# Kernel optimization log

Hardware: AMD Instinct MI355X
Metric: run time of the kernel (lower is better)

The kernel has to match this reference:

```python
import jax, jax.numpy as jnp
import numpy as np

VOCAB = 50257
D_EMB = 128
HIDDEN = 256
N_CLS = 2
B, T = 256, 2048


def setup_inputs() -> dict:
    key = jax.random.key(0)
    ks = jax.random.split(key, 8)
    batch = jax.random.randint(ks[0], (B, T), 0, VOCAB, dtype=jnp.int64) if jax.config.jax_enable_x64 else jax.random.randint(ks[0], (B, T), 0, VOCAB, dtype=jnp.int32)
    emb_table = jax.random.normal(ks[1], (VOCAB, D_EMB), dtype=jnp.float32) * 0.02
    emb_table = emb_table.at[0].set(0.0)  # padding_idx=0
    sx = 1.0 / np.sqrt(D_EMB)
    sh = 1.0 / np.sqrt(HIDDEN)
    wx_w = jax.random.uniform(ks[2], (D_EMB, HIDDEN), jnp.float32, -sx, sx)
    wx_b = jax.random.uniform(ks[3], (HIDDEN,), jnp.float32, -sx, sx)
    wh_w = jax.random.uniform(ks[4], (HIDDEN, HIDDEN), jnp.float32, -sh, sh)
    wh_b = jax.random.uniform(ks[5], (HIDDEN,), jnp.float32, -sh, sh)
    clf_w = jax.random.uniform(ks[6], (HIDDEN, N_CLS), jnp.float32, -sh, sh)
    clf_b = jax.random.uniform(ks[7], (N_CLS,), jnp.float32, -sh, sh)
    return {"batch": batch, "emb_table": emb_table, "wx_w": wx_w, "wx_b": wx_b,
            "wh_w": wh_w, "wh_b": wh_b, "clf_w": clf_w, "clf_b": clf_b}


def reference(batch, emb_table, wx_w, wx_b, wh_w, wh_b, clf_w, clf_b):
    # emb: [B, T, D_EMB]
    emb = emb_table[batch]
    b, t, d = emb.shape
    h0 = jnp.zeros((b, wh_w.shape[0]), dtype=emb.dtype)
    # Precompute wx(x) for all timesteps in one big GEMM (same math,
    # hoists the time-invariant contraction out of the sequential loop).
    ax = jnp.einsum('btd,dh->bth', emb, wx_w) + wx_b  # [B, T, H]

    def step(h, a_t):
        h_new = jnp.tanh(a_t + h @ wh_w + wh_b)
        return h_new, None

    h_final, _ = jax.lax.scan(step, h0, jnp.swapaxes(ax, 0, 1))  # scan over T
    return h_final @ clf_w + clf_b  # [B, 2]
```

## Files before the change

kernel.cpp:

```cpp
#include <hip/hip_runtime.h>
#include <hip/hip_bf16.h>

#define VOCAB  50257
#define D_EMB  128
#define HID    256
#define N_CLS  2
#define BSZ    256
#define T_LEN  2048

__global__ __launch_bounds__(256)
void tabax_kernel(const float* __restrict__ emb,
                  const float* __restrict__ wxw,
                  const float* __restrict__ wxb,
                  const float* __restrict__ whb,
                  float* __restrict__ tab)
{
    const int j  = threadIdx.x;
    const int v0 = blockIdx.x * 32;
    const int rows = min(32, VOCAB - v0);

    __shared__ float ebuf[32 * D_EMB];
    for (int i = j; i < rows * D_EMB; i += 256)
        ebuf[i] = emb[(size_t)v0 * D_EMB + i];
    __syncthreads();

    float acc[32];
#pragma unroll
    for (int r = 0; r < 32; ++r) acc[r] = 0.f;

#pragma unroll 8
    for (int d = 0; d < D_EMB; ++d) {
        float wxv = wxw[d * HID + j];
#pragma unroll
        for (int r = 0; r < 32; ++r)
            acc[r] = fmaf(ebuf[r * D_EMB + d], wxv, acc[r]);
    }

    const float bb = wxb[j] + whb[j];
    for (int r = 0; r < rows; ++r)
        tab[(size_t)(v0 + r) * HID + j] = acc[r] + bb;
}

__device__ __forceinline__ float fast_tanh(float x) {
    float e2 = __expf(2.f * x);
    return 1.f - 2.f / (e2 + 1.f);
}

#define DPP_RADD(ACC, N)                                                    \
    asm("v_add_f32 %0, %0, %0 row_ror:" #N " row_mask:0xf bank_mask:0xf"    \
        : "+v"(ACC))

__global__ __launch_bounds__(1024, 1)
void rnn_main_kernel(const int*   __restrict__ batch,
                     const float* __restrict__ whw,
                     const float* __restrict__ clfw,
                     const float* __restrict__ clfb,
                     const float* __restrict__ ax_tab,
                     float*       __restrict__ out)
{
    const int b   = blockIdx.x;
    const int tid = threadIdx.x;
    const int kg  = tid & 15;
    const int cg  = tid >> 4;
    const int c0  = cg * 4;
    const int kb  = kg * 16;
    const int rot = (kg >> 2) & 3;
    const int q   = kg & 3;

    __shared__ float hbuf[2][HID];
    __shared__ float sbuf[2][HID];

    float W[4][4][4];
#pragma unroll
    for (int e = 0; e < 4; ++e) {
        const int swz = (e + rot) & 3;
#pragma unroll
        for (int m = 0; m < 4; ++m) {
            const int k = kb + swz * 4 + m;
            const float4 w4 = *(const float4*)&whw[(size_t)k * HID + c0];
            W[e][m][0] = w4.x; W[e][m][1] = w4.y;
            W[e][m][2] = w4.z; W[e][m][3] = w4.w;
        }
    }
#pragma unroll
    for (int e = 0; e < 4; ++e)
#pragma unroll
        for (int m = 0; m < 4; ++m)
            asm volatile("" : "+v"(W[e][m][0]), "+v"(W[e][m][1]),
                              "+v"(W[e][m][2]), "+v"(W[e][m][3]));

    int lds_off[4];
#pragma unroll
    for (int e = 0; e < 4; ++e) lds_off[e] = kg * 64 + ((e + rot) & 3) * 16;

    const int  mycol = c0 + q;
    const bool wr    = (kg < 4);

    if (tid < HID) hbuf[0][tid] = 0.f;

    const int* brow = batch + (size_t)b * T_LEN;
    const float* axp = ax_tab + mycol;
    int tok_n = brow[0];
    float axv = axp[(unsigned)tok_n * 256u];
    tok_n = brow[1];
    __syncthreads();

#define RNN_STEP(CUR, NXT, TT)                                              \
    {                                                                       \
        const int tok_nn = ((TT) + 2 < T_LEN) ? brow[(TT) + 2] : 0;         \
        const float ax_n = axp[(unsigned)tok_n * 256u];                     \
        float acc[4];                                                       \
        const char* hb = (const char*)&hbuf[CUR][0];                        \
        {                                        \
            const float4 h4 = *(const float4*)(hb + lds_off[0]);            \
            const float hm[4] = {h4.x, h4.y, h4.z, h4.w};                   \
            _Pragma("unroll")                                               \
            for (int i = 0; i < 4; ++i) acc[i] = hm[0] * W[0][0][i];        \
            _Pragma("unroll")                                               \
            for (int m = 1; m < 4; ++m)                                     \
                _Pragma("unroll")                                           \
                for (int i = 0; i < 4; ++i)                                 \
                    acc[i] = fmaf(hm[m], W[0][m][i], acc[i]);               \
        }                                                                   \
        _Pragma("unroll")                                                   \
        for (int e = 1; e < 4; ++e) {                                       \
            const float4 h4 = *(const float4*)(hb + lds_off[e]);            \
            const float hm[4] = {h4.x, h4.y, h4.z, h4.w};                   \
            _Pragma("unroll")                                               \
            for (int m = 0; m < 4; ++m)                                     \
                _Pragma("unroll")                                           \
                for (int i = 0; i < 4; ++i)                                 \
                    acc[i] = fmaf(hm[m], W[e][m][i], acc[i]);               \
        }                                                                   \
          \
        _Pragma("unroll")                                                   \
        for (int i = 0; i < 4; ++i) {                                       \
            DPP_RADD(acc[i], 8);                                            \
            DPP_RADD(acc[i], 4);                                            \
            DPP_RADD(acc[i], 2);                                            \
            DPP_RADD(acc[i], 1);                                            \
        }                                                                   \
                        \
        const float r01 = (q & 1) ? acc[1] : acc[0];                        \
        const float r23 = (q & 1) ? acc[3] : acc[2];                        \
        const float res = (q & 2) ? r23 : r01;                              \
        const float hnew = fast_tanh(res + axv);                            \
        if (wr) hbuf[NXT][mycol] = hnew;                                    \
        __syncthreads();                                                    \
        axv   = ax_n;                                                       \
        tok_n = tok_nn;                                                     \
    }

    for (int t = 0; t < T_LEN; t += 2) {
        RNN_STEP(0, 1, t)
        RNN_STEP(1, 0, t + 1)
    }
#undef RNN_STEP

    if (tid < HID) {
        const float h = hbuf[0][tid];
        sbuf[0][tid] = h * clfw[tid * N_CLS + 0];
        sbuf[1][tid] = h * clfw[tid * N_CLS + 1];
    }
    __syncthreads();
    if (tid < 64) {
        float v = sbuf[0][tid] + sbuf[0][tid + 64] +
                  sbuf[0][tid + 128] + sbuf[0][tid + 192];
#pragma unroll
        for (int off = 32; off > 0; off >>= 1) v += __shfl_xor(v, off);
        if (tid == 0) out[b * N_CLS + 0] = v + clfb[0];
    } else if (tid < 128) {
        const int l = tid - 64;
        float v = sbuf[1][l] + sbuf[1][l + 64] +
                  sbuf[1][l + 128] + sbuf[1][l + 192];
#pragma unroll
        for (int off = 32; off > 0; off >>= 1) v += __shfl_xor(v, off);
        if (l == 0) out[b * N_CLS + 1] = v + clfb[1];
    }
}

__global__ __launch_bounds__(512, 2)
void rnn_fallback_kernel(const int*   __restrict__ batch,
                         const float* __restrict__ emb,
                         const float* __restrict__ wxw,
                         const float* __restrict__ wxb,
                         const float* __restrict__ whw,
                         const float* __restrict__ whb,
                         const float* __restrict__ clfw,
                         const float* __restrict__ clfb,
                         float*       __restrict__ out)
{
    const int b    = blockIdx.x;
    const int tid  = threadIdx.x;
    const int j    = tid >> 1;
    const int half = tid & 1;
    const int k0   = half * 128;

    __shared__ float hbuf[2][HID];
    __shared__ float ebuf[2][D_EMB];

    float w[128];
#pragma unroll
    for (int k = 0; k < 128; ++k)
        w[k] = whw[(size_t)(k0 + k) * HID + j];

    float wx[64];
#pragma unroll
    for (int d = 0; d < 64; ++d)
        wx[d] = wxw[(size_t)(half * 64 + d) * HID + j];

    const float bj  = whb[j];
    const float axb = wxb[j];

    if (tid < HID) hbuf[0][tid] = 0.f;

    const int* brow = batch + (size_t)b * T_LEN;

    int tok_n = brow[0];
    if (tid < D_EMB) ebuf[0][tid] = emb[(size_t)tok_n * D_EMB + tid];
    tok_n = brow[1];
    __syncthreads();

    float h_j = 0.f;
    int cur = 0;
    for (int t = 0; t < T_LEN; ++t) {
        const int nxt = cur ^ 1;
        const int tok_nn = (t + 2 < T_LEN) ? brow[t + 2] : 0;
        float ev = 0.f;
        if (t + 1 < T_LEN && tid < D_EMB)
            ev = emb[(size_t)tok_n * D_EMB + tid];

        float a0 = 0.f, a1 = 0.f, a2 = 0.f, a3 = 0.f;
        const float4* hv = (const float4*)&hbuf[cur][k0];
#pragma unroll
        for (int i = 0; i < 32; ++i) {
            float4 h4 = hv[i];
            a0 = fmaf(h4.x, w[4 * i + 0], a0);
            a1 = fmaf(h4.y, w[4 * i + 1], a1);
            a2 = fmaf(h4.z, w[4 * i + 2], a2);
            a3 = fmaf(h4.w, w[4 * i + 3], a3);
        }
        const float4* evv = (const float4*)&ebuf[cur][half * 64];
#pragma unroll
        for (int i = 0; i < 16; ++i) {
            float4 e4 = evv[i];
            a0 = fmaf(e4.x, wx[4 * i + 0], a0);
            a1 = fmaf(e4.y, wx[4 * i + 1], a1);
            a2 = fmaf(e4.z, wx[4 * i + 2], a2);
            a3 = fmaf(e4.w, wx[4 * i + 3], a3);
        }
        float s = (a0 + a1) + (a2 + a3);
        s += __shfl_xor(s, 1);

        h_j = fast_tanh(s + bj + axb);

        if (half == 0) hbuf[nxt][j] = h_j;
        if (t + 1 < T_LEN && tid < D_EMB) ebuf[nxt][tid] = ev;
        __syncthreads();

        tok_n = tok_nn;
        cur   = nxt;
    }

    if (half == 0) {
        hbuf[0][j] = h_j * clfw[j * N_CLS + 0];
        hbuf[1][j] = h_j * clfw[j * N_CLS + 1];
    }
    __syncthreads();
    if (tid < 64) {
        float v = hbuf[0][tid] + hbuf[0][tid + 64] +
                  hbuf[0][tid + 128] + hbuf[0][tid + 192];
#pragma unroll
        for (int off = 32; off > 0; off >>= 1) v += __shfl_xor(v, off);
        if (tid == 0) out[b * N_CLS + 0] = v + clfb[0];
    } else if (tid < 128) {
        const int l = tid - 64;
        float v = hbuf[1][l] + hbuf[1][l + 64] +
                  hbuf[1][l + 128] + hbuf[1][l + 192];
#pragma unroll
        for (int off = 32; off > 0; off >>= 1) v += __shfl_xor(v, off);
        if (l == 0) out[b * N_CLS + 1] = v + clfb[1];
    }
}

extern "C" void kernel_launch(void* const* d_in, const int* in_sizes, int n_in,
                              void* d_out, int out_size, void* d_ws, size_t ws_size,
                              hipStream_t stream)
{
    const int*   batch = (const int*)  d_in[0];
    const float* emb   = (const float*)d_in[1];
    const float* wxw   = (const float*)d_in[2];
    const float* wxb   = (const float*)d_in[3];
    const float* whw   = (const float*)d_in[4];
    const float* whb   = (const float*)d_in[5];
    const float* clfw  = (const float*)d_in[6];
    const float* clfb  = (const float*)d_in[7];
    float* out = (float*)d_out;

    const size_t tab_bytes = (size_t)VOCAB * HID * sizeof(float);
    if (ws_size >= tab_bytes) {
        float* tab = (float*)d_ws;
        tabax_kernel<<<(VOCAB + 31) / 32, 256, 0, stream>>>(emb, wxw, wxb, whb, tab);
        rnn_main_kernel<<<BSZ, 1024, 0, stream>>>(batch, whw, clfw, clfb, tab, out);
    } else {
        rnn_fallback_kernel<<<BSZ, 512, 0, stream>>>(batch, emb, wxw, wxb, whw, whb,
                                                     clfw, clfb, out);
    }
}
```

Measured before the change: 1.367 ms.

## Split recurrent weights between LDS and registers to cut register pressure

The first 128 rows of the hidden-to-hidden weight matrix now live transposed in shared memory with a padded stride, and only the upper 128 rows stay in registers (32 floats per thread instead of 64). Each step reads weights for the lower half from LDS alongside the hidden state, and the k-slice per thread changes from swizzled 16-element blocks to contiguous 8-element blocks in each half. This frees VGPRs but adds LDS weight reads to every serial timestep, on the critical path, and the kernel now uses about 132 KB of LDS per block.

After: 2.072 ms. +51.6%, slower.

```diff
diff --git a/kernel.cpp b/kernel.cpp
--- a/kernel.cpp
+++ b/kernel.cpp
@@ -7,6 +7,7 @@
 #define N_CLS  2
 #define BSZ    256
 #define T_LEN  2048
+#define WSTR   132
 
 __global__ __launch_bounds__(256)
 void tabax_kernel(const float* __restrict__ emb,
@@ -63,35 +64,34 @@
     const int kg  = tid & 15;
     const int cg  = tid >> 4;
     const int c0  = cg * 4;
-    const int kb  = kg * 16;
-    const int rot = (kg >> 2) & 3;
     const int q   = kg & 3;
 
+    __shared__ float wlds[256 * WSTR];
     __shared__ float hbuf[2][HID];
     __shared__ float sbuf[2][HID];
 
-    float W[4][4][4];
-#pragma unroll
-    for (int e = 0; e < 4; ++e) {
-        const int swz = (e + rot) & 3;
-#pragma unroll
-        for (int m = 0; m < 4; ++m) {
-            const int k = kb + swz * 4 + m;
-            const float4 w4 = *(const float4*)&whw[(size_t)k * HID + c0];
-            W[e][m][0] = w4.x; W[e][m][1] = w4.y;
-            W[e][m][2] = w4.z; W[e][m][3] = w4.w;
-        }
-    }
-#pragma unroll
-    for (int e = 0; e < 4; ++e)
-#pragma unroll
-        for (int m = 0; m < 4; ++m)
-            asm volatile("" : "+v"(W[e][m][0]), "+v"(W[e][m][1]),
-                              "+v"(W[e][m][2]), "+v"(W[e][m][3]));
-
-    int lds_off[4];
-#pragma unroll
-    for (int e = 0; e < 4; ++e) lds_off[e] = kg * 64 + ((e + rot) & 3) * 16;
+    for (int idx = tid; idx < 256 * 128; idx += 1024) {
+        const int c = idx >> 7;
+        const int k = idx & 127;
+        wlds[c * WSTR + k] = whw[(size_t)k * HID + c];
+    }
+
+    float Wr[8][4];
+#pragma unroll
+    for (int i = 0; i < 8; ++i) {
+        const int k = 128 + kg * 8 + i;
+        const float4 w4 = *(const float4*)&whw[(size_t)k * HID + c0];
+        Wr[i][0] = w4.x; Wr[i][1] = w4.y; Wr[i][2] = w4.z; Wr[i][3] = w4.w;
+    }
+#pragma unroll
+    for (int i = 0; i < 8; ++i)
+        asm volatile("" : "+v"(Wr[i][0]), "+v"(Wr[i][1]),
+                          "+v"(Wr[i][2]), "+v"(Wr[i][3]));
+
+    const float* wl[4];
+#pragma unroll
+    for (int cc = 0; cc < 4; ++cc)
+        wl[cc] = &wlds[(c0 + cc) * WSTR + kg * 8];
 
     const int  mycol = c0 + q;
     const bool wr    = (kg < 4);
@@ -109,29 +109,34 @@
     {                                                                       \
         const int tok_nn = ((TT) + 2 < T_LEN) ? brow[(TT) + 2] : 0;         \
         const float ax_n = axp[(unsigned)tok_n * 256u];                     \
+               \
+        const float4 hL0 = *(const float4*)&hbuf[CUR][kg * 8];              \
+        const float4 hL1 = *(const float4*)&hbuf[CUR][kg * 8 + 4];          \
+        const float4 hU0 = *(const float4*)&hbuf[CUR][128 + kg * 8];        \
+        const float4 hU1 = *(const float4*)&hbuf[CUR][128 + kg * 8 + 4];    \
         float acc[4];                                                       \
-        const char* hb = (const char*)&hbuf[CUR][0];                        \
-        {                                        \
-            const float4 h4 = *(const float4*)(hb + lds_off[0]);            \
-            const float hm[4] = {h4.x, h4.y, h4.z, h4.w};                   \
+        _Pragma("unroll")                                                   \
+        for (int cc = 0; cc < 4; ++cc) {                                    \
+            const float4 w0 = *(const float4*)(wl[cc]);                     \
+            const float4 w1 = *(const float4*)(wl[cc] + 4);                 \
+            float a;                                                        \
+            a = hL0.x * w0.x;                                               \
+            a = fmaf(hL0.y, w0.y, a);                                       \
+            a = fmaf(hL0.z, w0.z, a);                                       \
+            a = fmaf(hL0.w, w0.w, a);                                       \
+            a = fmaf(hL1.x, w1.x, a);                                       \
+            a = fmaf(hL1.y, w1.y, a);                                       \
+            a = fmaf(hL1.z, w1.z, a);                                       \
+            a = fmaf(hL1.w, w1.w, a);                                       \
+            acc[cc] = a;                                                    \
+        }                                                                   \
+        const float hu[8] = {hU0.x, hU0.y, hU0.z, hU0.w,                    \
+                             hU1.x, hU1.y, hU1.z, hU1.w};                   \
+        _Pragma("unroll")                                                   \
+        for (int i = 0; i < 8; ++i)                                         \
             _Pragma("unroll")                                               \
-            for (int i = 0; i < 4; ++i) acc[i] = hm[0] * W[0][0][i];        \
-            _Pragma("unroll")                                               \
-            for (int m = 1; m < 4; ++m)                                     \
-                _Pragma("unroll")                                           \
-                for (int i = 0; i < 4; ++i)                                 \
-                    acc[i] = fmaf(hm[m], W[0][m][i], acc[i]);               \
-        }                                                                   \
-        _Pragma("unroll")                                                   \
-        for (int e = 1; e < 4; ++e) {                                       \
-            const float4 h4 = *(const float4*)(hb + lds_off[e]);            \
-            const float hm[4] = {h4.x, h4.y, h4.z, h4.w};                   \
-            _Pragma("unroll")                                               \
-            for (int m = 0; m < 4; ++m)                                     \
-                _Pragma("unroll")                                           \
-                for (int i = 0; i < 4; ++i)                                 \
-                    acc[i] = fmaf(hm[m], W[e][m][i], acc[i]);               \
-        }                                                                   \
+            for (int cc = 0; cc < 4; ++cc)                                  \
+                acc[cc] = fmaf(hu[i], Wr[i][cc], acc[cc]);                  \
           \
         _Pragma("unroll")                                                   \
         for (int i = 0; i < 4; ++i) {                                       \
```
